# Performance work log

Measured on AMD Instinct MI355X. Metric: run time of the kernel, lower is better.

The kernel has to match this reference:

```python
import jax, jax.numpy as jnp
import numpy as np

N = 2048
NODE_DIM = 128
HID = 128
HID2 = max(HID // 2, 4)  # 64
NUM_EDGE_TYPES = 1
TEMPERATURE = 1.0
LN_EPS = 1e-5


def setup_inputs() -> dict:
    key = jax.random.key(0)
    ks = jax.random.split(key, 12)
    s = lambda fan_in: 1.0 / np.sqrt(fan_in)
    inp = {
        "node_features": jax.random.normal(ks[0], (N, NODE_DIM), dtype=jnp.float32),
        # node_transform: Linear(node_dim, hidden)
        "Wt": jax.random.uniform(ks[1], (NODE_DIM, HID), jnp.float32, -s(NODE_DIM), s(NODE_DIM)),
        "bt": jax.random.uniform(ks[2], (HID,), jnp.float32, -s(NODE_DIM), s(NODE_DIM)),
        # edge_mlp Linear(2*hidden, hidden)
        "W1": jax.random.uniform(ks[3], (2 * HID, HID), jnp.float32, -s(2 * HID), s(2 * HID)),
        "b1": jax.random.uniform(ks[4], (HID,), jnp.float32, -s(2 * HID), s(2 * HID)),
        # LayerNorm(hidden)
        "ln_g": jnp.ones((HID,), jnp.float32),
        "ln_b": jnp.zeros((HID,), jnp.float32),
        # Linear(hidden, hidden//2)
        "W2": jax.random.uniform(ks[5], (HID, HID2), jnp.float32, -s(HID), s(HID)),
        "b2": jax.random.uniform(ks[6], (HID2,), jnp.float32, -s(HID), s(HID)),
        # Linear(hidden//2, num_edge_types)
        "W3": jax.random.uniform(ks[7], (HID2, NUM_EDGE_TYPES), jnp.float32, -s(HID2), s(HID2)),
        "b3": jax.random.uniform(ks[8], (NUM_EDGE_TYPES,), jnp.float32, -s(HID2), s(HID2)),
    }
    return inp


def reference(node_features, Wt, bt, W1, b1, ln_g, ln_b, W2, b2, W3, b3):
    n = node_features.shape[0]
    # node transform + relu: [n, hid]
    h = jax.nn.relu(node_features @ Wt + bt)
    # upper-triangular pair indices (i < j), matching the python loop order
    idx_i, idx_j = jnp.triu_indices(n, k=1)
    # gather + concat: [n_pairs, 2*hid]
    pair_feats = jnp.concatenate([h[idx_i], h[idx_j]], axis=1)
    # MLP: linear -> LN -> relu -> (dropout=identity in eval) -> linear -> relu -> linear
    z = pair_feats @ W1 + b1
    mu = jnp.mean(z, axis=-1, keepdims=True)
    var = jnp.mean((z - mu) ** 2, axis=-1, keepdims=True)
    z = (z - mu) * jax.lax.rsqrt(var + LN_EPS) * ln_g + ln_b
    z = jax.nn.relu(z)
    z = jax.nn.relu(z @ W2 + b2)
    logits = z @ W3 + b3  # [n_pairs, 1]
    probs = jax.nn.sigmoid(logits / max(1e-6, TEMPERATURE))
    pair_index = jnp.stack([idx_i, idx_j], axis=0)  # [2, n_pairs]
    p = probs.squeeze(1)
    soft_adj = jnp.zeros((n, n), dtype=probs.dtype)
    soft_adj = soft_adj.at[idx_i, idx_j].set(p).at[idx_j, idx_i].set(p)
    return probs, pair_index, soft_adj
```

## Files before the change

kernel.cpp:

```cpp
#include <hip/hip_runtime.h>
#include <math.h>

#define NN 2048
#define HID 128
#define HID2 64
#define NP ((NN*(NN-1))/2)

typedef _Float16 f16x8 __attribute__((ext_vector_type(8)));
typedef float    f32x4 __attribute__((ext_vector_type(4)));
typedef float    f32x2 __attribute__((ext_vector_type(2)));

__global__ __launch_bounds__(128) void precompute_AB(
    const float* __restrict__ X, const float* __restrict__ Wt, const float* __restrict__ bt,
    const float* __restrict__ W1, const float* __restrict__ b1,
    _Float16* __restrict__ Ah, _Float16* __restrict__ Bp,
    float2* __restrict__ sa, float2* __restrict__ sb)
{
    __shared__ float x_s[HID];
    __shared__ float h_s[HID];
    __shared__ float red[2][4];
    const int row = blockIdx.x;
    const int c = threadIdx.x;
    x_s[c] = X[row*HID + c];
    __syncthreads();
    float hc = bt[c];
    #pragma unroll 8
    for (int k = 0; k < HID; ++k) hc = fmaf(x_s[k], Wt[k*HID + c], hc);
    h_s[c] = fmaxf(hc, 0.f);
    __syncthreads();
    float a = b1[c];
    float bsum = 0.f;
    #pragma unroll 8
    for (int k = 0; k < HID; ++k) {
        float hk = h_s[k];
        a    = fmaf(hk, W1[k*HID + c], a);
        bsum = fmaf(hk, W1[(HID + k)*HID + c], bsum);
    }
    const _Float16 ah = (_Float16)a;
    const _Float16 bh = (_Float16)bsum;
    Ah[row*HID + c] = ah;
    {
        const int ks = c >> 5, g4 = (c >> 3) & 3, e = c & 7;
        Bp[(((size_t)(row >> 4)*4 + ks)*64 + g4*16 + (row & 15))*8 + e] = bh;
    }
    const float ar = (float)ah;
    const float br = (float)bh;
    float r0 = ar, r1 = ar*ar, r2 = br, r3 = br*br;
    #pragma unroll
    for (int m = 1; m <= 32; m <<= 1) {
        r0 += __shfl_xor(r0, m); r1 += __shfl_xor(r1, m);
        r2 += __shfl_xor(r2, m); r3 += __shfl_xor(r3, m);
    }
    if ((c & 63) == 0) {
        red[c >> 6][0] = r0; red[c >> 6][1] = r1; red[c >> 6][2] = r2; red[c >> 6][3] = r3;
    }
    __syncthreads();
    if (c == 0) {
        sa[row] = make_float2(red[0][0] + red[1][0], red[0][1] + red[1][1]);
        sb[row] = make_float2(red[0][2] + red[1][2], red[0][3] + red[1][3]);
    }
}

__global__ __launch_bounds__(256) void pack_W2(const float* __restrict__ W2,
                                               const float* __restrict__ ln_g,
                                               const float* __restrict__ ln_b,
                                               _Float16* __restrict__ W2p,
                                               _Float16* __restrict__ ghl,
                                               _Float16* __restrict__ lhl)
{
    const int t = threadIdx.x;
    if (t < HID) { ghl[t] = (_Float16)ln_g[t]; lhl[t] = (_Float16)ln_b[t]; }
    for (int fs = t; fs < 16*64; fs += 256) {
        const int frag = fs >> 6, lane = fs & 63;
        const int ks = frag >> 2, nt = frag & 3;
        const int kbase = ks*32 + (lane >> 4)*8;
        const int col   = nt*16 + (lane & 15);
        #pragma unroll
        for (int e = 0; e < 8; ++e)
            W2p[fs*8 + e] = (_Float16)W2[(kbase + e)*HID2 + col];
    }
}

__global__ __launch_bounds__(256, 3) void pairs_mfma(
    const _Float16* __restrict__ Ah, const _Float16* __restrict__ Bp,
    const float2* __restrict__ sa, const float2* __restrict__ sb,
    const _Float16* __restrict__ ghl, const _Float16* __restrict__ lhl,
    const _Float16* __restrict__ W2p, const float* __restrict__ b2,
    const float* __restrict__ W3, const float* __restrict__ b3,
    float* __restrict__ out)
{
    __shared__ f16x8 w2s[16*64];

    {
        const f16x8* __restrict__ W2v = (const f16x8*)W2p;
        #pragma unroll
        for (int t = 0; t < 4; ++t)
            w2s[t*256 + threadIdx.x] = W2v[t*256 + threadIdx.x];
    }

    int t = blockIdx.x;
    int q = 0, base = 0;
    while (q < 7 && t >= base + 256*(8 - q)) { base += 256*(8 - q); ++q; }
    const int idx = t - base;
    const int den = 8 - q;
    const int i  = (q << 8) + idx / den;
    const int jb = q + idx % den;

    __syncthreads();

    const int w    = threadIdx.x >> 6;
    const int lane = threadIdx.x & 63;
    const int jw0  = (jb << 8) + (w << 6);
    if (jw0 + 63 < i) return;

    const int p16 = lane & 15;
    const int g4  = lane >> 4;

    f16x8 abf[4], gh[4], lh[4];
    #pragma unroll
    for (int ks = 0; ks < 4; ++ks) {
        const int kb = ks*32 + g4*8;
        abf[ks] = *(const f16x8*)(Ah + (size_t)i*HID + kb);
        gh[ks]  = *(const f16x8*)(ghl + kb);
        lh[ks]  = *(const f16x8*)(lhl + kb);
    }
    const float2 sav = sa[i];

    const f16x8* __restrict__ Bpv = (const f16x8*)Bp;

    float parts[4];

    f16x8 bcur[4], bnxt[4];
    {
        const size_t fb = ((size_t)(jw0 >> 4))*4;
        #pragma unroll
        for (int ks = 0; ks < 4; ++ks) bcur[ks] = Bpv[(fb + ks)*64 + lane];
    }
    f32x4 dc[4];
    #pragma unroll
    for (int c = 0; c < 4; ++c) {
        dc[c] = (f32x4){0.f,0.f,0.f,0.f};
        dc[c] = __builtin_amdgcn_mfma_f32_16x16x32_f16(abf[c], bcur[c], dc[c], 0, 0, 0);
    }

    #pragma unroll
    for (int s = 0; s < 4; ++s) {
        if (s < 3) {
            const size_t fbn = ((size_t)((jw0 + (s+1)*16) >> 4))*4;
            #pragma unroll
            for (int ks = 0; ks < 4; ++ks) bnxt[ks] = Bpv[(fbn + ks)*64 + lane];
        }
        const int j16 = jw0 + s*16;

        const float2 sbv = sb[j16 + p16];
        const float dd   = (dc[0][0] + dc[1][0]) + (dc[2][0] + dc[3][0]);
        const float mu   = (sav.x + sbv.x) * (1.f/HID);
        const float ez2  = (sav.y + sbv.y + 2.f*dd) * (1.f/HID);
        const float rstd = rsqrtf(ez2 - mu*mu + 1e-5f);
        const float v    = -mu * rstd;

        f32x4 dn[4];
        if (s < 3) {
            #pragma unroll
            for (int c = 0; c < 4; ++c) {
                dn[c] = (f32x4){0.f,0.f,0.f,0.f};
                dn[c] = __builtin_amdgcn_mfma_f32_16x16x32_f16(abf[c], bnxt[c], dn[c], 0, 0, 0);
            }
        }

        const _Float16 rh = (_Float16)rstd;
        const _Float16 vh = (_Float16)v;
        const f16x8 zero8 = {};

        f32x4 acc[4];
        #pragma unroll
        for (int nt = 0; nt < 4; ++nt) acc[nt] = *(const f32x4*)(b2 + nt*16 + g4*4);

        #pragma unroll
        for (int ks = 0; ks < 4; ++ks) {
            f16x8 z  = abf[ks] + bcur[ks];
            f16x8 qq = z * rh + vh;
            f16x8 af = __builtin_elementwise_max(gh[ks] * qq + lh[ks], zero8);
            #pragma unroll
            for (int nt = 0; nt < 4; ++nt)
                acc[nt] = __builtin_amdgcn_mfma_f32_16x16x32_f16(w2s[(ks*4 + nt)*64 + lane], af, acc[nt], 0, 0, 0);
        }

        f32x2 pv = (f32x2){0.f, 0.f};
        const f32x2 z2 = (f32x2){0.f, 0.f};
        #pragma unroll
        for (int nt = 0; nt < 4; ++nt) {
            const f32x2* w3p = (const f32x2*)(W3 + nt*16 + g4*4);
            f32x2 a0 = (f32x2){acc[nt][0], acc[nt][1]};
            f32x2 a1 = (f32x2){acc[nt][2], acc[nt][3]};
            pv = __builtin_elementwise_max(a0, z2) * w3p[0] + pv;
            pv = __builtin_elementwise_max(a1, z2) * w3p[1] + pv;
        }
        float part = pv[0] + pv[1];
        part += __shfl_xor(part, 16);
        part += __shfl_xor(part, 32);
        parts[s] = part;

        if (s < 3) {
            #pragma unroll
            for (int ks = 0; ks < 4; ++ks) bcur[ks] = bnxt[ks];
            #pragma unroll
            for (int c = 0; c < 4; ++c) dc[c] = dn[c];
        }
    }

    const int sq = lane >> 4;
    float x = parts[0];
    x = (sq == 1) ? parts[1] : x;
    x = (sq == 2) ? parts[2] : x;
    x = (sq == 3) ? parts[3] : x;

    float* probs = out;
    float* pi    = out + NP;
    float* adj   = out + 3*(size_t)NP;
    const int j = jw0 + lane;
    if (j == i) {
        adj[(size_t)i*NN + i] = 0.f;
    } else if (j > i) {
        const float pr = 1.f / (1.f + __expf(-(x + b3[0])));
        const int kpair = i*(NN-1) - (i*(i-1))/2 + (j - i - 1);
        probs[kpair]    = pr;
        pi[kpair]       = (float)i;
        pi[NP + kpair]  = (float)j;
        adj[(size_t)i*NN + j] = pr;
        adj[(size_t)j*NN + i] = pr;
    }
}

extern "C" void kernel_launch(void* const* d_in, const int* in_sizes, int n_in,
                              void* d_out, int out_size, void* d_ws, size_t ws_size,
                              hipStream_t stream) {
    const float* X    = (const float*)d_in[0];
    const float* Wt   = (const float*)d_in[1];
    const float* bt   = (const float*)d_in[2];
    const float* W1   = (const float*)d_in[3];
    const float* b1   = (const float*)d_in[4];
    const float* ln_g = (const float*)d_in[5];
    const float* ln_b = (const float*)d_in[6];
    const float* W2   = (const float*)d_in[7];
    const float* b2   = (const float*)d_in[8];
    const float* W3   = (const float*)d_in[9];
    const float* b3   = (const float*)d_in[10];
    float* out = (float*)d_out;

    float2*    sa  = (float2*)d_ws;
    float2*    sb  = sa + NN;
    _Float16*  Ah  = (_Float16*)(sb + NN);
    _Float16*  Bp  = Ah + (size_t)NN * HID;
    _Float16*  W2p = Bp + (size_t)NN * HID;
    _Float16*  ghl = W2p + 16*64*8;
    _Float16*  lhl = ghl + HID;

    precompute_AB<<<NN, HID, 0, stream>>>(X, Wt, bt, W1, b1, Ah, Bp, sa, sb);
    pack_W2<<<1, 256, 0, stream>>>(W2, ln_g, ln_b, W2p, ghl, lhl);

    const int nblk = 256 * 36;
    pairs_mfma<<<nblk, 256, 0, stream>>>(Ah, Bp, sa, sb, ghl, lhl, W2p, b2, W3, b3, out);
}
```

Before: 96.12 us.

## Keep W2 fragments in registers instead of LDS and drop B prefetch

Removes the shared-memory W2 staging and the block barrier, and instead has each wave load all 16 W2 fragments directly into registers from global memory. It also removes the software pipelining of B-tile loads and the dot-product MFMAs, loading each tile inside the loop. Launch bounds drop from 3 to 2 blocks per SM to give the extra register room. This trades LDS reads and the sync for higher register pressure, lower occupancy and less overlap of loads with compute.

```diff
diff --git a/kernel.cpp b/kernel.cpp
--- a/kernel.cpp
+++ b/kernel.cpp
@@ -81,7 +81,7 @@
     }
 }
 
-__global__ __launch_bounds__(256, 3) void pairs_mfma(
+__global__ __launch_bounds__(256, 2) void pairs_mfma(
     const _Float16* __restrict__ Ah, const _Float16* __restrict__ Bp,
     const float2* __restrict__ sa, const float2* __restrict__ sb,
     const _Float16* __restrict__ ghl, const _Float16* __restrict__ lhl,
@@ -89,15 +89,6 @@
     const float* __restrict__ W3, const float* __restrict__ b3,
     float* __restrict__ out)
 {
-    __shared__ f16x8 w2s[16*64];
-
-    {
-        const f16x8* __restrict__ W2v = (const f16x8*)W2p;
-        #pragma unroll
-        for (int t = 0; t < 4; ++t)
-            w2s[t*256 + threadIdx.x] = W2v[t*256 + threadIdx.x];
-    }
-
     int t = blockIdx.x;
     int q = 0, base = 0;
     while (q < 7 && t >= base + 256*(8 - q)) { base += 256*(8 - q); ++q; }
@@ -106,8 +97,6 @@
     const int i  = (q << 8) + idx / den;
     const int jb = q + idx % den;
 
-    __syncthreads();
-
     const int w    = threadIdx.x >> 6;
     const int lane = threadIdx.x & 63;
     const int jw0  = (jb << 8) + (w << 6);
@@ -115,6 +104,11 @@
 
     const int p16 = lane & 15;
     const int g4  = lane >> 4;
+
+    const f16x8* __restrict__ W2v = (const f16x8*)W2p;
+    f16x8 w2r[16];
+    #pragma unroll
+    for (int f = 0; f < 16; ++f) w2r[f] = W2v[f*64 + lane];
 
     f16x8 abf[4], gh[4], lh[4];
     #pragma unroll
@@ -130,43 +124,30 @@
 
     float parts[4];
 
-    f16x8 bcur[4], bnxt[4];
-    {
-        const size_t fb = ((size_t)(jw0 >> 4))*4;
+    #pragma unroll
+    for (int s = 0; s < 4; ++s) {
+        const int j16 = jw0 + s*16;
+
+        f16x8 bcur[4];
+        const size_t fb = ((size_t)(j16 >> 4))*4;
         #pragma unroll
         for (int ks = 0; ks < 4; ++ks) bcur[ks] = Bpv[(fb + ks)*64 + lane];
-    }
-    f32x4 dc[4];
-    #pragma unroll
-    for (int c = 0; c < 4; ++c) {
-        dc[c] = (f32x4){0.f,0.f,0.f,0.f};
-        dc[c] = __builtin_amdgcn_mfma_f32_16x16x32_f16(abf[c], bcur[c], dc[c], 0, 0, 0);
-    }
-
-    #pragma unroll
-    for (int s = 0; s < 4; ++s) {
-        if (s < 3) {
-            const size_t fbn = ((size_t)((jw0 + (s+1)*16) >> 4))*4;
-            #pragma unroll
-            for (int ks = 0; ks < 4; ++ks) bnxt[ks] = Bpv[(fbn + ks)*64 + lane];
-        }
-        const int j16 = jw0 + s*16;
+
+        f32x4 d0 = (f32x4){0.f,0.f,0.f,0.f};
+        f32x4 d1 = (f32x4){0.f,0.f,0.f,0.f};
+        f32x4 d2 = (f32x4){0.f,0.f,0.f,0.f};
+        f32x4 d3 = (f32x4){0.f,0.f,0.f,0.f};
+        d0 = __builtin_amdgcn_mfma_f32_16x16x32_f16(abf[0], bcur[0], d0, 0, 0, 0);
+        d1 = __builtin_amdgcn_mfma_f32_16x16x32_f16(abf[1], bcur[1], d1, 0, 0, 0);
+        d2 = __builtin_amdgcn_mfma_f32_16x16x32_f16(abf[2], bcur[2], d2, 0, 0, 0);
+        d3 = __builtin_amdgcn_mfma_f32_16x16x32_f16(abf[3], bcur[3], d3, 0, 0, 0);
 
         const float2 sbv = sb[j16 + p16];
-        const float dd   = (dc[0][0] + dc[1][0]) + (dc[2][0] + dc[3][0]);
+        const float dd   = (d0[0] + d1[0]) + (d2[0] + d3[0]);
         const float mu   = (sav.x + sbv.x) * (1.f/HID);
         const float ez2  = (sav.y + sbv.y + 2.f*dd) * (1.f/HID);
         const float rstd = rsqrtf(ez2 - mu*mu + 1e-5f);
         const float v    = -mu * rstd;
-
-        f32x4 dn[4];
-        if (s < 3) {
-            #pragma unroll
-            for (int c = 0; c < 4; ++c) {
-                dn[c] = (f32x4){0.f,0.f,0.f,0.f};
-                dn[c] = __builtin_amdgcn_mfma_f32_16x16x32_f16(abf[c], bnxt[c], dn[c], 0, 0, 0);
-            }
-        }
 
         const _Float16 rh = (_Float16)rstd;
         const _Float16 vh = (_Float16)v;
@@ -183,7 +164,7 @@
             f16x8 af = __builtin_elementwise_max(gh[ks] * qq + lh[ks], zero8);
             #pragma unroll
             for (int nt = 0; nt < 4; ++nt)
-                acc[nt] = __builtin_amdgcn_mfma_f32_16x16x32_f16(w2s[(ks*4 + nt)*64 + lane], af, acc[nt], 0, 0, 0);
+                acc[nt] = __builtin_amdgcn_mfma_f32_16x16x32_f16(w2r[ks*4 + nt], af, acc[nt], 0, 0, 0);
         }
 
         f32x2 pv = (f32x2){0.f, 0.f};
@@ -200,13 +181,6 @@
         part += __shfl_xor(part, 16);
         part += __shfl_xor(part, 32);
         parts[s] = part;
-
-        if (s < 3) {
-            #pragma unroll
-            for (int ks = 0; ks < 4; ++ks) bcur[ks] = bnxt[ks];
-            #pragma unroll
-            for (int c = 0; c < 4; ++c) dc[c] = dn[c];
-        }
     }
 
     const int sq = lane >> 4;
```

Measured after the change: 113.8 us. 18.4% more time.
